# Optimization experiments

Measured on AMD Instinct MI355X. Metric: run time of the kernel, lower is better.

The kernel has to match this reference:

```python
import jax, jax.numpy as jnp
import numpy as np

N = 4096
M = 1024
APPERTURE = 250
L1, L2, L3, PRED = 1024, 512, 128, 1
EPS = 1e-6


def _layer_norm(x, gamma, beta):
    # torch x.std(-1) is unbiased (ddof=1)
    mean = jnp.mean(x, axis=-1, keepdims=True)
    std = jnp.std(x, axis=-1, ddof=1, keepdims=True)
    return gamma * (x - mean) / (std + EPS) + beta


def _self_attention(x, Wq, Wk, Wv, Wo, band_mask):
    # x: [n, m]; Linear(bias=False) => x @ W.T
    K = x @ Wk.T
    Q = (x @ Wq.T) * 0.06
    V = x @ Wv.T
    logits = Q @ K.T                      # [n, n]
    logits = jnp.where(band_mask, logits, -jnp.inf)  # keep |i-j| < apperture
    att = jax.nn.softmax(logits, axis=-1)
    # original: y = (V^T @ att)^T == att^T @ V  (note the transpose!)
    y = att.T @ V
    return y @ Wo.T, att


def setup_inputs() -> dict:
    key = jax.random.key(0)
    ks = jax.random.split(key, 20)
    s = 0.02
    inp = {
        'x1': jax.random.normal(ks[0], (1, N, M), jnp.float32),
        'x2': jax.random.normal(ks[1], (1, N, M), jnp.float32),
        'x3': jax.random.normal(ks[2], (1, N, M), jnp.float32),
        'Wq': jax.random.normal(ks[3], (M, M), jnp.float32) * s,
        'Wk': jax.random.normal(ks[4], (M, M), jnp.float32) * s,
        'Wv': jax.random.normal(ks[5], (M, M), jnp.float32) * s,
        'Wo': jax.random.normal(ks[6], (M, M), jnp.float32) * s,
        'ka_w': jax.random.normal(ks[7], (L1, M), jnp.float32) * s,
        'ka_b': jnp.zeros((L1,), jnp.float32),
        'kb_w': jax.random.normal(ks[8], (L2, L1), jnp.float32) * s,
        'kb_b': jnp.zeros((L2,), jnp.float32),
        'kc_w': jax.random.normal(ks[9], (L3, L2), jnp.float32) * s,
        'kc_b': jnp.zeros((L3,), jnp.float32),
        'kd_w': jax.random.normal(ks[10], (PRED, L3), jnp.float32) * s,
        'kd_b': jnp.zeros((PRED,), jnp.float32),
        'g13': jnp.ones((M,), jnp.float32),
        'b13': jnp.zeros((M,), jnp.float32),
        'gkc': jnp.ones((L3,), jnp.float32),
        'bkc': jnp.zeros((L3,), jnp.float32),
        'seq_len': N,
    }
    return inp


def reference(x1, x2, x3, Wq, Wk, Wv, Wo, ka_w, ka_b, kb_w, kb_b, kc_w, kc_b,
              kd_w, kd_b, g13, b13, gkc, bkc, seq_len):
    x1 = x1.reshape(-1, x1.shape[2])
    x2 = x2.reshape(-1, x2.shape[2])
    x3 = x3.reshape(-1, x3.shape[2])
    n = x1.shape[0]
    idx = jnp.arange(n)
    band_mask = jnp.abs(idx[:, None] - idx[None, :]) < APPERTURE  # allowed

    y1, att1 = _self_attention(x1, Wq, Wk, Wv, Wo, band_mask)
    y2, _ = _self_attention(x2, Wq, Wk, Wv, Wo, band_mask)
    y3, _ = _self_attention(x3, Wq, Wk, Wv, Wo, band_mask)

    # residual + (dropout == identity in eval) + shared LayerNorm
    y1 = _layer_norm(y1 + x1, g13, b13)
    y2 = _layer_norm(y2 + x2, g13, b13)
    y3 = _layer_norm(y3 + x3, g13, b13)

    y = y1 + y2 + y3  # cmb == [1,1,1]
    y = y @ ka_w.T + ka_b
    y = y @ kb_w.T + kb_b
    y = jax.nn.relu(y @ kc_w.T + kc_b)
    y = _layer_norm(y, gkc, bkc)
    y = jax.nn.sigmoid(y @ kd_w.T + kd_b)
    return y.reshape(1, -1), att1
```

## Files before the change

### kernel.cpp

```cpp
#include <hip/hip_runtime.h>
#include <hip/hip_bf16.h>
#include <cstdint>
#include <cstddef>

#define NSEQ 4096
#define MDIM 1024

typedef __attribute__((ext_vector_type(8))) short short8;
typedef __attribute__((ext_vector_type(4))) float f32x4;
typedef __attribute__((ext_vector_type(2))) long long2v;
typedef __attribute__((ext_vector_type(8))) int int8v;
typedef __attribute__((ext_vector_type(4))) int int4v;

typedef const __attribute__((address_space(1))) void gvoid_t;
typedef __attribute__((address_space(3))) void lvoid_t;

__device__ __forceinline__ unsigned short f2b(float x) {
  union { float f; unsigned int u; } a; a.f = x;
  unsigned int r = (a.u + 0x7fffu + ((a.u >> 16) & 1u)) >> 16;
  return (unsigned short)r;
}
__device__ __forceinline__ float b2f(unsigned short u) {
  union { float f; unsigned int u32; } a; a.u32 = ((unsigned int)u) << 16;
  return a.f;
}
__device__ __forceinline__ unsigned char f2e4(float x) {
  return (unsigned char)(__builtin_amdgcn_cvt_pk_fp8_f32(x, x, 0, false) & 0xff);
}
__device__ __forceinline__ unsigned int f2e4x4(float a, float b, float c, float d) {
  unsigned int lo = __builtin_amdgcn_cvt_pk_fp8_f32(a, b, 0, false);
  return (unsigned int)__builtin_amdgcn_cvt_pk_fp8_f32(c, d, lo, true);
}

__device__ __forceinline__ int8v pack32(const unsigned char* p0,
                                        const unsigned char* p1) {
  int4v lo = *(const int4v*)p0;
  int4v hi = *(const int4v*)p1;
  int8v r;
  r[0] = lo[0]; r[1] = lo[1]; r[2] = lo[2]; r[3] = lo[3];
  r[4] = hi[0]; r[5] = hi[1]; r[6] = hi[2]; r[7] = hi[3];
  return r;
}

__device__ __forceinline__ void xcd_decode(int bid, int& bx, int& by) {
  int slot = bid >> 3;
  bx = (bid & 7) * 12 + slot % 12;
  by = slot / 12;
}

__global__ __launch_bounds__(256) void k_cvt_all(
    const float* __restrict__ s0, const float* __restrict__ s1,
    const float* __restrict__ s2, const float* __restrict__ s3,
    const float* __restrict__ s4, const float* __restrict__ s5,
    const float* __restrict__ s6,
    const float* __restrict__ xa, const float* __restrict__ xb,
    const float* __restrict__ xc,
    unsigned char* __restrict__ Wf8, unsigned short* __restrict__ Wmlp,
    unsigned char* __restrict__ Xdst, float* __restrict__ sums) {
  int idx = blockIdx.x * 256 + threadIdx.x;
  if (idx < 1048576) {
    int seg = idx >> 18, local = idx & 262143;
    const float* src = (seg == 0) ? s0 : (seg == 1) ? s1 : (seg == 2) ? s2 : s3;
    float4 v = *(const float4*)(src + (size_t)local * 4);
    *(unsigned int*)(Wf8 + (size_t)idx * 4) =
        f2e4x4(v.x * 64.f, v.y * 64.f, v.z * 64.f, v.w * 64.f);
  } else if (idx < 1458176) {
    int i2 = idx - 1048576;
    const float* src; int local;
    if (i2 < 262144) { src = s4; local = i2; }
    else if (i2 < 393216) { src = s5; local = i2 - 262144; }
    else { src = s6; local = i2 - 393216; }
    float4 v = *(const float4*)(src + (size_t)local * 4);
    ushort4 o; o.x = f2b(v.x); o.y = f2b(v.y); o.z = f2b(v.z); o.w = f2b(v.w);
    *(ushort4*)(Wmlp + (size_t)i2 * 4) = o;
  } else if (idx < 4603904) {
    int i2 = idx - 1458176;
    int seg = i2 >> 20, local = i2 & 1048575;
    const float* src = (seg == 0) ? xa : (seg == 1) ? xb : xc;
    float4 v = *(const float4*)(src + (size_t)local * 4);
    *(unsigned int*)(Xdst + (size_t)i2 * 4) = f2e4x4(v.x, v.y, v.z, v.w);
  } else {
    int i3 = idx - 4603904;
    *(float4*)(sums + (size_t)i3 * 4) = make_float4(0.f, 0.f, 0.f, 0.f);
  }
}

template <int MODE, int OKIND, int DO_EXP>
__device__ __forceinline__ void gemm_core256(
    int bx, int by,
    const unsigned char* __restrict__ A, int lda,
    const unsigned char* __restrict__ B, int ldb,
    void* __restrict__ Cout, void* __restrict__ Cout2, int ldc,
    int K, float alpha,
    const unsigned char* __restrict__ A1, const unsigned char* __restrict__ A2,
    float* __restrict__ sums_out, unsigned char* __restrict__ smem) {
  const unsigned char* Ab;
  const unsigned char* Bb;
  void* Cdst = Cout;
  int ldce = ldc;
  int rbase, cbase;
  int ldae = lda, ldbe = ldb;
  if constexpr (MODE == 0) {
    Ab = A + (size_t)by * 128 * lda;
    Bb = B + (size_t)bx * 128 * ldb;
    rbase = bx * 128; cbase = by * 128;
  } else if constexpr (MODE == 3) {
    if (by < 16) {
      Ab = A + (size_t)by * 128 * lda;
      Bb = B + (size_t)bx * 128 * ldb;
      if (by >= 8) Cdst = Cout2;
      rbase = bx * 128; cbase = (by & 7) * 128;
    } else {
      Ab = B + (size_t)bx * 128 * ldb;
      Bb = A1 + (size_t)(by - 16) * 128 * 1024;
      Cdst = (void*)const_cast<unsigned char*>(A2);
      rbase = (by - 16) * 128; cbase = bx * 128;
      ldce = 3 * NSEQ;
    }
  } else {
    int s = bx >> 5, ti = bx & 31;
    int bt = ti + by - 2;
    Ab = A + (size_t)(s * 32 + bt) * 128 * lda;
    Bb = B + (size_t)bx * 128 * ldb;
    rbase = bx * 128; cbase = by * 128;
  }

  const int t = threadIdx.x;
  const int l = t & 63;
  const int w = t >> 6;
  const int fr = l & 15;
  const int quad = l >> 4;
  const int wm = (w >> 1) * 64;
  const int wn = (w & 1) * 64;
  const int fq4 = quad * 4;

  int srow[8], scg[8], sloff[8];
#pragma unroll
  for (int j = 0; j < 8; j++) {
    srow[j] = w * 32 + j * 4 + (l >> 4);
    scg[j] = ((l & 15) - srow[j]) & 15;
    sloff[j] = (w * 32 + j * 4) * 256 + l * 16;
  }

  unsigned char* As = smem;
  unsigned char* Bs = smem + 32768;

  f32x4 acc[4][4];
#pragma unroll
  for (int m = 0; m < 4; m++)
#pragma unroll
    for (int n = 0; n < 4; n++) acc[m][n] = (f32x4){0.f, 0.f, 0.f, 0.f};

  const int nt = K >> 8;
  for (int tt = 0; tt < nt; tt++) {
    int kk = tt * 256;
    __syncthreads();
#pragma unroll
    for (int j = 0; j < 8; j++)
      __builtin_amdgcn_global_load_lds(
          (gvoid_t*)(Ab + (size_t)srow[j] * ldae + kk + scg[j] * 16),
          (lvoid_t*)(As + sloff[j]), 16, 0, 0);
#pragma unroll
    for (int j = 0; j < 8; j++)
      __builtin_amdgcn_global_load_lds(
          (gvoid_t*)(Bb + (size_t)srow[j] * ldbe + kk + scg[j] * 16),
          (lvoid_t*)(Bs + sloff[j]), 16, 0, 0);
    __syncthreads();
#pragma unroll
    for (int h = 0; h < 2; h++) {
      const int cb = h * 8 + quad * 2;
      int8v a8[4], b8[4];
#pragma unroll
      for (int m = 0; m < 4; m++) {
        int r = wm + m * 16 + fr;
        int s0i = (cb + r) & 15, s1i = (cb + 1 + r) & 15;
        a8[m] = pack32(As + r * 256 + s0i * 16, As + r * 256 + s1i * 16);
      }
#pragma unroll
      for (int n = 0; n < 4; n++) {
        int r = wn + n * 16 + fr;
        int s0i = (cb + r) & 15, s1i = (cb + 1 + r) & 15;
        b8[n] = pack32(Bs + r * 256 + s0i * 16, Bs + r * 256 + s1i * 16);
      }
#pragma unroll
      for (int m = 0; m < 4; m++)
#pragma unroll
        for (int n = 0; n < 4; n++)
          acc[m][n] = __builtin_amdgcn_mfma_scale_f32_16x16x128_f8f6f4(
              a8[m], b8[n], acc[m][n], 0, 0, 0, 0x7F7F7F7F, 0, 0x7F7F7F7F);
    }
  }

  float rowsum[4] = {0.f, 0.f, 0.f, 0.f};
  const int jb = ((bx & 31) - 2) * 128;
#pragma unroll
  for (int m = 0; m < 4; m++) {
#pragma unroll
    for (int n = 0; n < 4; n++) {
      int oc = cbase + wm + m * 16 + fq4;
      int orow = rbase + wn + n * 16 + fr;
      float v0 = acc[m][n][0] * alpha, v1 = acc[m][n][1] * alpha;
      float v2 = acc[m][n][2] * alpha, v3 = acc[m][n][3] * alpha;
      if constexpr (OKIND == 1) {
        if constexpr (DO_EXP) {
          v0 = __expf(v0); v1 = __expf(v1); v2 = __expf(v2); v3 = __expf(v3);
          if constexpr (MODE == 1) {
            int d0 = (orow & 4095) - (jb + oc);
            rowsum[n] += ((unsigned)(d0 + 249) < 499u ? v0 : 0.f)
                       + ((unsigned)(d0 + 248) < 499u ? v1 : 0.f)
                       + ((unsigned)(d0 + 247) < 499u ? v2 : 0.f)
                       + ((unsigned)(d0 + 246) < 499u ? v3 : 0.f);
          }
        }
        ushort4 o; o.x = f2b(v0); o.y = f2b(v1); o.z = f2b(v2); o.w = f2b(v3);
        *(uint2*)((unsigned short*)Cdst + (size_t)orow * ldce + oc) = *(uint2*)&o;
      } else {
        *(unsigned int*)((unsigned char*)Cdst + (size_t)orow * ldce + oc) =
            f2e4x4(v0, v1, v2, v3);
      }
    }
  }
  if constexpr (MODE == 1 && DO_EXP) {
#pragma unroll
    for (int n = 0; n < 4; n++) {
      float sv = rowsum[n];
      sv += __shfl_xor(sv, 16);
      sv += __shfl_xor(sv, 32);
      if (quad == 0) {
        int orow = rbase + wn + n * 16 + fr;
        atomicAdd(sums_out + orow, sv);
      }
    }
  }
}

__device__ __forceinline__ void gemm_core_av(
    int bx, int by,
    const unsigned char* __restrict__ A, int lda,
    const unsigned char* __restrict__ B,
    void* __restrict__ Cout, int ldc, float alpha,
    const unsigned char* __restrict__ A1, const unsigned char* __restrict__ A2,
    unsigned char* __restrict__ smem) {
  int s = bx >> 5, ti = bx & 31;
  const unsigned char* Ab = A + (size_t)by * 128 * lda + s * NSEQ;
  const unsigned char* Bbase = (s == 0) ? B : ((s == 1) ? A1 : A2);
  const unsigned char* Bb = Bbase + (size_t)ti * 128 * 640;
  const int ldbe = 640;
  int lo = ti - 2; if (lo < 0) lo = 0;
  int hi = ti + 3; if (hi > 32) hi = 32;
  int k0 = lo * 128, k1 = hi * 128;
  int b_koff = (ti - 2) * 128;
  int rbase = bx * 128, cbase = by * 128;

  const int t = threadIdx.x;
  const int l = t & 63;
  const int w = t >> 6;
  const int fr = l & 15;
  const int quad = l >> 4;
  const int wm = (w >> 1) * 64;
  const int wn = (w & 1) * 64;
  const int fq4 = quad * 4;

  int srow[4], scg[4], sloff[4];
#pragma unroll
  for (int j = 0; j < 4; j++) {
    srow[j] = w * 32 + j * 8 + (l >> 3);
    scg[j] = ((l & 7) - srow[j]) & 7;
    sloff[j] = (w * 32 + j * 8) * 128 + l * 16;
  }

  f32x4 acc[4][4];
#pragma unroll
  for (int m = 0; m < 4; m++)
#pragma unroll
    for (int n = 0; n < 4; n++) acc[m][n] = (f32x4){0.f, 0.f, 0.f, 0.f};

  const int c0 = quad * 2;
  const int nt = (k1 - k0) >> 7;

  {
    int kk = k0, kb = kk - b_koff;
#pragma unroll
    for (int j = 0; j < 4; j++)
      __builtin_amdgcn_global_load_lds(
          (gvoid_t*)(Ab + (size_t)srow[j] * lda + kk + scg[j] * 16),
          (lvoid_t*)(smem + sloff[j]), 16, 0, 0);
#pragma unroll
    for (int j = 0; j < 4; j++)
      __builtin_amdgcn_global_load_lds(
          (gvoid_t*)(Bb + (size_t)srow[j] * ldbe + kb + scg[j] * 16),
          (lvoid_t*)(smem + 16384 + sloff[j]), 16, 0, 0);
  }

  for (int tt = 0; tt < nt; tt++) {
    if (tt + 1 < nt) {
      int kk = k0 + (tt + 1) * 128, kb = kk - b_koff;
      unsigned char* Asn = smem + ((tt + 1) & 1) * 32768;
#pragma unroll
      for (int j = 0; j < 4; j++)
        __builtin_amdgcn_global_load_lds(
            (gvoid_t*)(Ab + (size_t)srow[j] * lda + kk + scg[j] * 16),
            (lvoid_t*)(Asn + sloff[j]), 16, 0, 0);
#pragma unroll
      for (int j = 0; j < 4; j++)
        __builtin_amdgcn_global_load_lds(
            (gvoid_t*)(Bb + (size_t)srow[j] * ldbe + kb + scg[j] * 16),
            (lvoid_t*)(Asn + 16384 + sloff[j]), 16, 0, 0);
      __builtin_amdgcn_sched_barrier(0);
      asm volatile("s_waitcnt vmcnt(8)" ::: "memory");
    } else {
      asm volatile("s_waitcnt vmcnt(0)" ::: "memory");
    }
    asm volatile("s_barrier" ::: "memory");

    const unsigned char* Asc = smem + (tt & 1) * 32768;
    const unsigned char* Bsc = Asc + 16384;
    int8v a8[4], b8[4];
#pragma unroll
    for (int m = 0; m < 4; m++) {
      int r = wm + m * 16 + fr;
      int s0i = (c0 + r) & 7, s1i = (s0i + 1) & 7;
      a8[m] = pack32(Asc + r * 128 + s0i * 16, Asc + r * 128 + s1i * 16);
    }
#pragma unroll
    for (int n = 0; n < 4; n++) {
      int r = wn + n * 16 + fr;
      int s0i = (c0 + r) & 7, s1i = (s0i + 1) & 7;
      b8[n] = pack32(Bsc + r * 128 + s0i * 16, Bsc + r * 128 + s1i * 16);
    }
#pragma unroll
    for (int m = 0; m < 4; m++)
#pragma unroll
      for (int n = 0; n < 4; n++)
        acc[m][n] = __builtin_amdgcn_mfma_scale_f32_16x16x128_f8f6f4(
            a8[m], b8[n], acc[m][n], 0, 0, 0, 0x7F7F7F7F, 0, 0x7F7F7F7F);
    asm volatile("s_barrier" ::: "memory");
  }

#pragma unroll
  for (int m = 0; m < 4; m++) {
#pragma unroll
    for (int n = 0; n < 4; n++) {
      int oc = cbase + wm + m * 16 + fq4;
      int orow = rbase + wn + n * 16 + fr;
      float v0 = acc[m][n][0] * alpha, v1 = acc[m][n][1] * alpha;
      float v2 = acc[m][n][2] * alpha, v3 = acc[m][n][3] * alpha;
      *(unsigned int*)((unsigned char*)Cout + (size_t)orow * ldc + oc) =
          f2e4x4(v0, v1, v2, v3);
    }
  }
}

__global__ __launch_bounds__(256) void k_qkv(
    const unsigned char* __restrict__ A, const unsigned char* __restrict__ B,
    void* __restrict__ Cout, void* __restrict__ Cout2, float alpha,
    const unsigned char* __restrict__ A1, const unsigned char* __restrict__ A2) {
  __shared__ unsigned char smem[2 * 128 * 256];
  int bx, by; xcd_decode(blockIdx.x, bx, by);
  gemm_core256<3, 2, 0>(bx, by, A, 1024, B, 1024, Cout, Cout2, 1024, 1024, alpha,
                        A1, A2, nullptr, smem);
}

__global__ __launch_bounds__(256) void k_logits(
    const unsigned char* __restrict__ A, const unsigned char* __restrict__ B,
    void* __restrict__ Cout, float alpha, float* __restrict__ sums) {
  int bx, by; xcd_decode(blockIdx.x, bx, by);
  int ti = bx & 31;
  int bt = ti + by - 2;
  if (bt < 0 || bt >= 32) return;
  __shared__ unsigned char smem[2 * 128 * 256];
  gemm_core256<1, 1, 1>(bx, by, A, 1024, B, 1024, Cout, nullptr, 640, 1024, alpha,
                        nullptr, nullptr, sums, smem);
}

__global__ __launch_bounds__(256) void k_av(
    const unsigned char* __restrict__ A, const unsigned char* __restrict__ B,
    void* __restrict__ Cout, float alpha,
    const unsigned char* __restrict__ A1, const unsigned char* __restrict__ A2) {
  __shared__ unsigned char smem[4 * 128 * 128];
  int bx, by; xcd_decode(blockIdx.x, bx, by);
  gemm_core_av(bx, by, A, 3 * NSEQ, B, Cout, 1024, alpha, A1, A2, smem);
}

__global__ __launch_bounds__(256) void k_wo(
    const unsigned char* __restrict__ A, const unsigned char* __restrict__ B,
    void* __restrict__ Cout, float alpha) {
  __shared__ unsigned char smem[2 * 128 * 256];
  int bx, by; xcd_decode(blockIdx.x, bx, by);
  gemm_core256<0, 1, 0>(bx, by, A, 1024, B, 1024, Cout, nullptr, 1024, 1024, alpha,
                        nullptr, nullptr, nullptr, smem);
}

__global__ __launch_bounds__(256) void k_gemm64(
    const unsigned short* __restrict__ A, int lda,
    const unsigned short* __restrict__ B, int ldb,
    void* __restrict__ Cout, int ldc, int K,
    const float* __restrict__ bias, int relu, int out_bf16) {
  __shared__ unsigned short smem[4 * 64 * 64];
  int bx = blockIdx.x, by = blockIdx.y;
  const unsigned short* Ab = A + (size_t)by * 64 * lda;
  const unsigned short* Bb = B + (size_t)bx * 64 * ldb;
  int rbase = bx * 64, cbase = by * 64;

  const int t = threadIdx.x;
  const int l = t & 63;
  const int w = t >> 6;
  const int fr = l & 15;
  const int quad = l >> 4;
  const int wm = (w & 1) * 32;
  const int wn = (w >> 1) * 32;
  const int fq4 = quad * 4;

  int srow[2], scg[2], sloff[2];
#pragma unroll
  for (int j = 0; j < 2; j++) {
    srow[j] = w * 16 + j * 8 + (l >> 3);
    scg[j] = ((l & 7) - srow[j]) & 7;
    sloff[j] = (w * 16 + j * 8) * 64 + l * 8;
  }

  f32x4 acc[2][2];
#pragma unroll
  for (int m = 0; m < 2; m++)
#pragma unroll
    for (int n = 0; n < 2; n++) acc[m][n] = (f32x4){0.f, 0.f, 0.f, 0.f};

  const int nt = K >> 6;

#pragma unroll
  for (int j = 0; j < 2; j++)
    __builtin_amdgcn_global_load_lds(
        (gvoid_t*)(Ab + (size_t)srow[j] * lda + scg[j] * 8),
        (lvoid_t*)(smem + sloff[j]), 16, 0, 0);
#pragma unroll
  for (int j = 0; j < 2; j++)
    __builtin_amdgcn_global_load_lds(
        (gvoid_t*)(Bb + (size_t)srow[j] * ldb + scg[j] * 8),
        (lvoid_t*)(smem + 4096 + sloff[j]), 16, 0, 0);

  for (int tt = 0; tt < nt; tt++) {
    __syncthreads();
    if (tt + 1 < nt) {
      int kk = (tt + 1) * 64;
      unsigned short* Asn = smem + ((tt + 1) & 1) * 8192;
#pragma unroll
      for (int j = 0; j < 2; j++)
        __builtin_amdgcn_global_load_lds(
            (gvoid_t*)(Ab + (size_t)srow[j] * lda + kk + scg[j] * 8),
            (lvoid_t*)(Asn + sloff[j]), 16, 0, 0);
#pragma unroll
      for (int j = 0; j < 2; j++)
        __builtin_amdgcn_global_load_lds(
            (gvoid_t*)(Bb + (size_t)srow[j] * ldb + kk + scg[j] * 8),
            (lvoid_t*)(Asn + 4096 + sloff[j]), 16, 0, 0);
    }
    const unsigned short* Asc = smem + (tt & 1) * 8192;
    const unsigned short* Bsc = Asc + 4096;
#pragma unroll
    for (int s = 0; s < 2; s++) {
      short8 af[2], bf[2];
#pragma unroll
      for (int m = 0; m < 2; m++) {
        int r = wm + m * 16 + fr;
        int slot = (s * 4 + quad + r) & 7;
        af[m] = *(const short8*)(Asc + r * 64 + slot * 8);
      }
#pragma unroll
      for (int n = 0; n < 2; n++) {
        int r = wn + n * 16 + fr;
        int slot = (s * 4 + quad + r) & 7;
        bf[n] = *(const short8*)(Bsc + r * 64 + slot * 8);
      }
#pragma unroll
      for (int m = 0; m < 2; m++)
#pragma unroll
        for (int n = 0; n < 2; n++)
          acc[m][n] = __builtin_amdgcn_mfma_f32_16x16x32_bf16(af[m], bf[n], acc[m][n], 0, 0, 0);
    }
  }

#pragma unroll
  for (int m = 0; m < 2; m++) {
#pragma unroll
    for (int n = 0; n < 2; n++) {
      int oc = cbase + wm + m * 16 + fq4;
      int orow = rbase + wn + n * 16 + fr;
      float4 bv = bias ? *(const float4*)(bias + oc) : make_float4(0.f, 0.f, 0.f, 0.f);
      float v0 = acc[m][n][0] + bv.x, v1 = acc[m][n][1] + bv.y;
      float v2 = acc[m][n][2] + bv.z, v3 = acc[m][n][3] + bv.w;
      if (relu) {
        v0 = fmaxf(v0, 0.f); v1 = fmaxf(v1, 0.f);
        v2 = fmaxf(v2, 0.f); v3 = fmaxf(v3, 0.f);
      }
      if (out_bf16) {
        ushort4 o; o.x = f2b(v0); o.y = f2b(v1); o.z = f2b(v2); o.w = f2b(v3);
        *(uint2*)((unsigned short*)Cout + (size_t)orow * ldc + oc) = *(uint2*)&o;
      } else {
        *(float4*)((float*)Cout + (size_t)orow * ldc + oc) = make_float4(v0, v1, v2, v3);
      }
    }
  }
}

__global__ __launch_bounds__(256) void k_attw(const unsigned short* __restrict__ Eband,
                                              const float* __restrict__ sums,
                                              unsigned char* __restrict__ t0,
                                              unsigned char* __restrict__ t1,
                                              unsigned char* __restrict__ t2,
                                              float* __restrict__ att) {
  __shared__ unsigned char T[128][132];
  int bid = blockIdx.x;
  if (bid < 480) {
    int tjoff = bid % 5;
    int byy = bid / 5;
    int s = byy >> 5, ti = byy & 31;
    int tj = ti + tjoff - 2;
    if (tj < 0 || tj >= 32) return;
    unsigned char* dst = (s == 0) ? t0 : ((s == 1) ? t1 : t2);
    int t = threadIdx.x;
    int c0 = (ti - tj + 2) * 128;
    int colg = (t & 31) * 4;
    for (int jj = t >> 5; jj < 128; jj += 8) {
      int jg = s * NSEQ + tj * 128 + jj;
      float inv = 16.f / sums[jg];
      ushort4 v = *(const ushort4*)&Eband[(size_t)jg * 640 + c0 + colg];
      float vv[4] = {b2f(v.x), b2f(v.y), b2f(v.z), b2f(v.w)};
#pragma unroll
      for (int q = 0; q < 4; q++) {
        int i = ti * 128 + colg + q;
        int d = i - (tj * 128 + jj);
        float a = (d < 250 && d > -250) ? vv[q] * inv : 0.f;
        T[colg + q][jj] = f2e4(a);
      }
    }
    __syncthreads();
    int jb0 = (tj - ti + 2) * 128;
    for (int ii = t >> 5; ii < 128; ii += 8) {
      size_t o = (size_t)(ti * 128 + ii) * 640 + jb0 + colg;
      *(unsigned int*)(dst + o) = *(const unsigned int*)&T[ii][colg];
    }
  } else {
    int i = bid - 480;
    int ti = i >> 7, cbase = (ti - 2) * 128;
    int jlo = i - 249; if (jlo < 0) jlo = 0;
    int jhi = i + 249; if (jhi > NSEQ - 1) jhi = NSEQ - 1;
    float inv = 1.f / sums[i];
    const unsigned short* L = Eband + (size_t)i * 640;
    float* arow = att + (size_t)i * NSEQ;
    for (int j0 = threadIdx.x * 4; j0 < NSEQ; j0 += 1024) {
      float ov[4];
#pragma unroll
      for (int q = 0; q < 4; q++) {
        int j = j0 + q;
        ov[q] = (j >= jlo && j <= jhi) ? b2f(L[j - cbase]) * inv : 0.f;
      }
      *(float4*)(arow + j0) = make_float4(ov[0], ov[1], ov[2], ov[3]);
    }
  }
}

__global__ __launch_bounds__(256) void k_ln3(const unsigned short* __restrict__ yo,
                                             const float* __restrict__ x1,
                                             const float* __restrict__ x2,
                                             const float* __restrict__ x3,
                                             const float* __restrict__ g,
                                             const float* __restrict__ b,
                                             unsigned short* __restrict__ ysum_b) {
  int i = blockIdx.x, t = threadIdx.x;
  int w = t >> 6, lane = t & 63;
  __shared__ float red[8];
  const float* xs[3] = {x1, x2, x3};
  float4 gg = *(const float4*)(g + t * 4);
  float4 bb = *(const float4*)(b + t * 4);
  float acc[4] = {0.f, 0.f, 0.f, 0.f};
  for (int s = 0; s < 3; s++) {
    ushort4 yv = *(const ushort4*)(yo + ((size_t)(s * NSEQ + i)) * MDIM + t * 4);
    float4 xx = *(const float4*)(xs[s] + (size_t)i * MDIM + t * 4);
    float v[4] = {b2f(yv.x) + xx.x, b2f(yv.y) + xx.y, b2f(yv.z) + xx.z, b2f(yv.w) + xx.w};
    float s1 = v[0] + v[1] + v[2] + v[3];
    float s2 = v[0]*v[0] + v[1]*v[1] + v[2]*v[2] + v[3]*v[3];
    for (int off = 32; off; off >>= 1) { s1 += __shfl_xor(s1, off); s2 += __shfl_xor(s2, off); }
    __syncthreads();
    if (lane == 0) { red[w] = s1; red[4 + w] = s2; }
    __syncthreads();
    float S1 = red[0] + red[1] + red[2] + red[3];
    float S2 = red[4] + red[5] + red[6] + red[7];
    float mean = S1 * (1.f / 1024.f);
    float var = (S2 - S1 * mean) * (1.f / 1023.f);
    float rstd = 1.f / (sqrtf(var) + 1e-6f);
    acc[0] += gg.x * (v[0] - mean) * rstd + bb.x;
    acc[1] += gg.y * (v[1] - mean) * rstd + bb.y;
    acc[2] += gg.z * (v[2] - mean) * rstd + bb.z;
    acc[3] += gg.w * (v[3] - mean) * rstd + bb.w;
  }
  ushort4 o;
  o.x = f2b(acc[0]); o.y = f2b(acc[1]); o.z = f2b(acc[2]); o.w = f2b(acc[3]);
  *(ushort4*)(ysum_b + (size_t)i * MDIM + t * 4) = o;
}

__global__ __launch_bounds__(128) void k_final(const float* __restrict__ h3,
                                               const float* __restrict__ g,
                                               const float* __restrict__ b,
                                               const float* __restrict__ kdw,
                                               const float* __restrict__ kdb,
                                               float* __restrict__ yout) {
  int i = blockIdx.x, t = threadIdx.x;
  float v = h3[(size_t)i * 128 + t];
  float s1 = v, s2 = v * v;
  for (int off = 32; off; off >>= 1) { s1 += __shfl_xor(s1, off); s2 += __shfl_xor(s2, off); }
  __shared__ float red[4];
  int w = t >> 6, lane = t & 63;
  if (lane == 0) { red[w] = s1; red[2 + w] = s2; }
  __syncthreads();
  float S1 = red[0] + red[1], S2 = red[2] + red[3];
  float mean = S1 * (1.f / 128.f);
  float var = (S2 - S1 * mean) * (1.f / 127.f);
  float rstd = 1.f / (sqrtf(var) + 1e-6f);
  float ln = g[t] * (v - mean) * rstd + b[t];
  float p = ln * kdw[t];
  for (int off = 32; off; off >>= 1) p += __shfl_xor(p, off);
  __syncthreads();
  if (lane == 0) red[w] = p;
  __syncthreads();
  if (t == 0) {
    float z = red[0] + red[1] + kdb[0];
    yout[i] = 1.f / (1.f + __expf(-z));
  }
}

extern "C" void kernel_launch(void* const* d_in, const int* in_sizes, int n_in,
                              void* d_out, int out_size, void* d_ws, size_t ws_size,
                              hipStream_t stream) {
  const float* x1 = (const float*)d_in[0];
  const float* x2 = (const float*)d_in[1];
  const float* x3 = (const float*)d_in[2];
  const float* Wq = (const float*)d_in[3];
  const float* Wk = (const float*)d_in[4];
  const float* Wv = (const float*)d_in[5];
  const float* Wo = (const float*)d_in[6];
  const float* ka_w = (const float*)d_in[7];
  const float* ka_b = (const float*)d_in[8];
  const float* kb_w = (const float*)d_in[9];
  const float* kb_b = (const float*)d_in[10];
  const float* kc_w = (const float*)d_in[11];
  const float* kc_b = (const float*)d_in[12];
  const float* kd_w = (const float*)d_in[13];
  const float* kd_b = (const float*)d_in[14];
  const float* g13 = (const float*)d_in[15];
  const float* b13 = (const float*)d_in[16];
  const float* gkc = (const float*)d_in[17];
  const float* bkc = (const float*)d_in[18];

  float* y_out = (float*)d_out;
  float* att_out = y_out + NSEQ;

  char* ws = (char*)d_ws;
  size_t off = 0;
  auto alloc = [&](size_t bytes) -> void* {
    void* p = ws + off;
    off += (bytes + 255) & ~(size_t)255;
    return p;
  };
  const size_t NM = (size_t)3 * NSEQ * MDIM;
  unsigned char* Wf = (unsigned char*)alloc(4 * 1048576);
  unsigned short* Wmlp = (unsigned short*)alloc((1048576 + 524288 + 65536) * 2);
  unsigned char* Xf = (unsigned char*)alloc(NM);
  unsigned char* Qf = (unsigned char*)alloc(NM);
  unsigned char* Kf = (unsigned char*)alloc(NM);
  unsigned char* VTf = (unsigned char*)alloc(NM);
  unsigned short* Eband = (unsigned short*)alloc((size_t)3 * NSEQ * 640 * 2);
  float* sums = (float*)alloc((size_t)3 * NSEQ * 4);
  unsigned char* aT0 = (unsigned char*)alloc((size_t)NSEQ * 640);
  unsigned char* aT1 = (unsigned char*)alloc((size_t)NSEQ * 640);
  unsigned char* aT2 = (unsigned char*)alloc((size_t)NSEQ * 640);
  unsigned char* Wv_f = Wf + 2097152;
  unsigned char* Wo_f = Wf + 3145728;
  unsigned short* ka_b16 = Wmlp;
  unsigned short* kb_b16 = Wmlp + 1048576;
  unsigned short* kc_b16 = Wmlp + 1572864;
  unsigned char* yb = Xf;
  unsigned short* yo = (unsigned short*)Qf;
  unsigned short* ysum_b = (unsigned short*)VTf;
  unsigned short* h1b = (unsigned short*)Xf;
  unsigned short* h2b = (unsigned short*)Qf;
  float* h3 = (float*)aT0;

  k_cvt_all<<<17996, 256, 0, stream>>>(Wq, Wk, Wv, Wo, ka_w, kb_w, kc_w,
                                       x1, x2, x3, Wf, Wmlp, Xf, sums);

  k_qkv<<<2304, 256, 0, stream>>>(Wf, Xf, Qf, Kf, 1.f / 64.f, Wv_f, VTf);
  k_logits<<<480, 256, 0, stream>>>(Kf, Qf, Eband, 0.06f, sums);
  k_attw<<<4576, 256, 0, stream>>>(Eband, sums, aT0, aT1, aT2, att_out);
  k_av<<<768, 256, 0, stream>>>(VTf, aT0, yb, 0.5f, aT1, aT2);
  k_wo<<<768, 256, 0, stream>>>(Wo_f, yb, yo, 1.f / 512.f);
  k_ln3<<<4096, 256, 0, stream>>>(yo, x1, x2, x3, g13, b13, ysum_b);

  k_gemm64<<<dim3(64, 16), 256, 0, stream>>>(ka_b16, 1024, ysum_b, 1024, h1b, 1024,
                                             1024, ka_b, 0, 1);
  k_gemm64<<<dim3(64, 8), 256, 0, stream>>>(kb_b16, 1024, h1b, 1024, h2b, 512,
                                            1024, kb_b, 0, 1);
  k_gemm64<<<dim3(64, 2), 256, 0, stream>>>(kc_b16, 512, h2b, 512, h3, 128,
                                            512, kc_b, 1, 0);
  k_final<<<4096, 128, 0, stream>>>(h3, gkc, bkc, kd_w, kd_b, y_out);
}
```

Measured before the change: 315.0 us.

## Fuse Q/K and V-pair projections into dual-accumulator kernel sharing the X tile

Replaces the generic QKV GEMM with a dedicated kernel where each block loads one X tile and two weight tiles (Wq+Wk, or two Wv row blocks), computing two output tiles with two accumulator sets. This halves the block count and reuses the shared X tile across two MFMA streams to cut global and LDS traffic. The MLP GEMM launches also get an XCD-aware block-index remap for better L2 locality. The cost is doubled accumulator registers, which may reduce occupancy, and a smaller K step (128) with more barriers.

```diff
diff --git a/kernel.cpp b/kernel.cpp
--- a/kernel.cpp
+++ b/kernel.cpp
@@ -85,44 +85,28 @@
   }
 }
 
-template <int MODE, int OKIND, int DO_EXP>
-__device__ __forceinline__ void gemm_core256(
-    int bx, int by,
-    const unsigned char* __restrict__ A, int lda,
-    const unsigned char* __restrict__ B, int ldb,
-    void* __restrict__ Cout, void* __restrict__ Cout2, int ldc,
-    int K, float alpha,
-    const unsigned char* __restrict__ A1, const unsigned char* __restrict__ A2,
-    float* __restrict__ sums_out, unsigned char* __restrict__ smem) {
-  const unsigned char* Ab;
-  const unsigned char* Bb;
-  void* Cdst = Cout;
-  int ldce = ldc;
-  int rbase, cbase;
-  int ldae = lda, ldbe = ldb;
-  if constexpr (MODE == 0) {
-    Ab = A + (size_t)by * 128 * lda;
-    Bb = B + (size_t)bx * 128 * ldb;
-    rbase = bx * 128; cbase = by * 128;
-  } else if constexpr (MODE == 3) {
-    if (by < 16) {
-      Ab = A + (size_t)by * 128 * lda;
-      Bb = B + (size_t)bx * 128 * ldb;
-      if (by >= 8) Cdst = Cout2;
-      rbase = bx * 128; cbase = (by & 7) * 128;
-    } else {
-      Ab = B + (size_t)bx * 128 * ldb;
-      Bb = A1 + (size_t)(by - 16) * 128 * 1024;
-      Cdst = (void*)const_cast<unsigned char*>(A2);
-      rbase = (by - 16) * 128; cbase = bx * 128;
-      ldce = 3 * NSEQ;
-    }
+__global__ __launch_bounds__(256) void k_qkv(
+    const unsigned char* __restrict__ W, const unsigned char* __restrict__ X,
+    unsigned char* __restrict__ Qf, unsigned char* __restrict__ Kf,
+    unsigned char* __restrict__ VT, float alpha) {
+  __shared__ unsigned char smem[3 * 128 * 128];
+  unsigned char* S  = smem;
+  unsigned char* U1 = smem + 16384;
+  unsigned char* U2 = smem + 32768;
+  int slot = blockIdx.x >> 3;
+  int bx = (blockIdx.x & 7) * 12 + slot % 12;
+  int by = slot / 12;
+  const bool qk = (by < 8);
+  const unsigned char* Sb = X + (size_t)bx * 128 * 1024;
+  const unsigned char* U1b;
+  const unsigned char* U2b;
+  if (qk) {
+    U1b = W + (size_t)by * 131072;
+    U2b = W + 1048576 + (size_t)by * 131072;
   } else {
-    int s = bx >> 5, ti = bx & 31;
-    int bt = ti + by - 2;
-    Ab = A + (size_t)(s * 32 + bt) * 128 * lda;
-    Bb = B + (size_t)bx * 128 * ldb;
-    rbase = bx * 128; cbase = by * 128;
+    int j = by - 8;
+    U1b = W + 2097152 + (size_t)j * 131072;
+    U2b = W + 2097152 + (size_t)(j + 4) * 131072;
   }
 
   const int t = threadIdx.x;
@@ -134,6 +118,187 @@
   const int wn = (w & 1) * 64;
   const int fq4 = quad * 4;
 
+  int srow[4], scg[4], sloff[4];
+#pragma unroll
+  for (int j = 0; j < 4; j++) {
+    srow[j] = w * 32 + j * 8 + (l >> 3);
+    scg[j] = ((l & 7) - srow[j]) & 7;
+    sloff[j] = (w * 32 + j * 8) * 128 + l * 16;
+  }
+
+  f32x4 acc1[4][4], acc2[4][4];
+#pragma unroll
+  for (int m = 0; m < 4; m++)
+#pragma unroll
+    for (int n = 0; n < 4; n++) {
+      acc1[m][n] = (f32x4){0.f, 0.f, 0.f, 0.f};
+      acc2[m][n] = (f32x4){0.f, 0.f, 0.f, 0.f};
+    }
+
+  const int c0 = quad * 2;
+  for (int tt = 0; tt < 8; tt++) {
+    int kk = tt * 128;
+    __syncthreads();
+#pragma unroll
+    for (int j = 0; j < 4; j++)
+      __builtin_amdgcn_global_load_lds(
+          (gvoid_t*)(Sb + (size_t)srow[j] * 1024 + kk + scg[j] * 16),
+          (lvoid_t*)(S + sloff[j]), 16, 0, 0);
+#pragma unroll
+    for (int j = 0; j < 4; j++)
+      __builtin_amdgcn_global_load_lds(
+          (gvoid_t*)(U1b + (size_t)srow[j] * 1024 + kk + scg[j] * 16),
+          (lvoid_t*)(U1 + sloff[j]), 16, 0, 0);
+#pragma unroll
+    for (int j = 0; j < 4; j++)
+      __builtin_amdgcn_global_load_lds(
+          (gvoid_t*)(U2b + (size_t)srow[j] * 1024 + kk + scg[j] * 16),
+          (lvoid_t*)(U2 + sloff[j]), 16, 0, 0);
+    __syncthreads();
+    if (qk) {
+      int8v b8[4];
+#pragma unroll
+      for (int n = 0; n < 4; n++) {
+        int r = wn + n * 16 + fr;
+        int s0i = (c0 + r) & 7, s1i = (s0i + 1) & 7;
+        b8[n] = pack32(S + r * 128 + s0i * 16, S + r * 128 + s1i * 16);
+      }
+      {
+        int8v a8[4];
+#pragma unroll
+        for (int m = 0; m < 4; m++) {
+          int r = wm + m * 16 + fr;
+          int s0i = (c0 + r) & 7, s1i = (s0i + 1) & 7;
+          a8[m] = pack32(U1 + r * 128 + s0i * 16, U1 + r * 128 + s1i * 16);
+        }
+#pragma unroll
+        for (int m = 0; m < 4; m++)
+#pragma unroll
+          for (int n = 0; n < 4; n++)
+            acc1[m][n] = __builtin_amdgcn_mfma_scale_f32_16x16x128_f8f6f4(
+                a8[m], b8[n], acc1[m][n], 0, 0, 0, 0x7F7F7F7F, 0, 0x7F7F7F7F);
+#pragma unroll
+        for (int m = 0; m < 4; m++) {
+          int r = wm + m * 16 + fr;
+          int s0i = (c0 + r) & 7, s1i = (s0i + 1) & 7;
+          a8[m] = pack32(U2 + r * 128 + s0i * 16, U2 + r * 128 + s1i * 16);
+        }
+#pragma unroll
+        for (int m = 0; m < 4; m++)
+#pragma unroll
+          for (int n = 0; n < 4; n++)
+            acc2[m][n] = __builtin_amdgcn_mfma_scale_f32_16x16x128_f8f6f4(
+                a8[m], b8[n], acc2[m][n], 0, 0, 0, 0x7F7F7F7F, 0, 0x7F7F7F7F);
+      }
+    } else {
+      int8v a8[4];
+#pragma unroll
+      for (int m = 0; m < 4; m++) {
+        int r = wm + m * 16 + fr;
+        int s0i = (c0 + r) & 7, s1i = (s0i + 1) & 7;
+        a8[m] = pack32(S + r * 128 + s0i * 16, S + r * 128 + s1i * 16);
+      }
+      {
+        int8v b8[4];
+#pragma unroll
+        for (int n = 0; n < 4; n++) {
+          int r = wn + n * 16 + fr;
+          int s0i = (c0 + r) & 7, s1i = (s0i + 1) & 7;
+          b8[n] = pack32(U1 + r * 128 + s0i * 16, U1 + r * 128 + s1i * 16);
+        }
+#pragma unroll
+        for (int m = 0; m < 4; m++)
+#pragma unroll
+          for (int n = 0; n < 4; n++)
+            acc1[m][n] = __builtin_amdgcn_mfma_scale_f32_16x16x128_f8f6f4(
+                a8[m], b8[n], acc1[m][n], 0, 0, 0, 0x7F7F7F7F, 0, 0x7F7F7F7F);
+#pragma unroll
+        for (int n = 0; n < 4; n++) {
+          int r = wn + n * 16 + fr;
+          int s0i = (c0 + r) & 7, s1i = (s0i + 1) & 7;
+          b8[n] = pack32(U2 + r * 128 + s0i * 16, U2 + r * 128 + s1i * 16);
+        }
+#pragma unroll
+        for (int m = 0; m < 4; m++)
+#pragma unroll
+          for (int n = 0; n < 4; n++)
+            acc2[m][n] = __builtin_amdgcn_mfma_scale_f32_16x16x128_f8f6f4(
+                a8[m], b8[n], acc2[m][n], 0, 0, 0, 0x7F7F7F7F, 0, 0x7F7F7F7F);
+      }
+    }
+  }
+
+  if (qk) {
+    int cbase = by * 128, rbase = bx * 128;
+#pragma unroll
+    for (int m = 0; m < 4; m++) {
+#pragma unroll
+      for (int n = 0; n < 4; n++) {
+        int oc = cbase + wm + m * 16 + fq4;
+        int orow = rbase + wn + n * 16 + fr;
+        *(unsigned int*)(Qf + (size_t)orow * 1024 + oc) =
+            f2e4x4(acc1[m][n][0] * alpha, acc1[m][n][1] * alpha,
+                   acc1[m][n][2] * alpha, acc1[m][n][3] * alpha);
+        *(unsigned int*)(Kf + (size_t)orow * 1024 + oc) =
+            f2e4x4(acc2[m][n][0] * alpha, acc2[m][n][1] * alpha,
+                   acc2[m][n][2] * alpha, acc2[m][n][3] * alpha);
+      }
+    }
+  } else {
+    int j = by - 8;
+    int cbase = bx * 128;
+    int rb1 = j * 128, rb2 = (j + 4) * 128;
+#pragma unroll
+    for (int m = 0; m < 4; m++) {
+#pragma unroll
+      for (int n = 0; n < 4; n++) {
+        int oc = cbase + wm + m * 16 + fq4;
+        int oro = wn + n * 16 + fr;
+        *(unsigned int*)(VT + (size_t)(rb1 + oro) * 12288 + oc) =
+            f2e4x4(acc1[m][n][0] * alpha, acc1[m][n][1] * alpha,
+                   acc1[m][n][2] * alpha, acc1[m][n][3] * alpha);
+        *(unsigned int*)(VT + (size_t)(rb2 + oro) * 12288 + oc) =
+            f2e4x4(acc2[m][n][0] * alpha, acc2[m][n][1] * alpha,
+                   acc2[m][n][2] * alpha, acc2[m][n][3] * alpha);
+      }
+    }
+  }
+}
+
+template <int MODE, int OKIND, int DO_EXP>
+__device__ __forceinline__ void gemm_core256(
+    int bx, int by,
+    const unsigned char* __restrict__ A, int lda,
+    const unsigned char* __restrict__ B, int ldb,
+    void* __restrict__ Cout, int ldc,
+    int K, float alpha,
+    float* __restrict__ sums_out, unsigned char* __restrict__ smem) {
+  const unsigned char* Ab;
+  const unsigned char* Bb;
+  int ldce = ldc;
+  int rbase, cbase;
+  int ldae = lda, ldbe = ldb;
+  if constexpr (MODE == 0) {
+    Ab = A + (size_t)by * 128 * lda;
+    Bb = B + (size_t)bx * 128 * ldb;
+    rbase = bx * 128; cbase = by * 128;
+  } else {
+    int s = bx >> 5, ti = bx & 31;
+    int bt = ti + by - 2;
+    Ab = A + (size_t)(s * 32 + bt) * 128 * lda;
+    Bb = B + (size_t)bx * 128 * ldb;
+    rbase = bx * 128; cbase = by * 128;
+  }
+
+  const int t = threadIdx.x;
+  const int l = t & 63;
+  const int w = t >> 6;
+  const int fr = l & 15;
+  const int quad = l >> 4;
+  const int wm = (w >> 1) * 64;
+  const int wn = (w & 1) * 64;
+  const int fq4 = quad * 4;
+
   int srow[8], scg[8], sloff[8];
 #pragma unroll
   for (int j = 0; j < 8; j++) {
@@ -201,23 +366,18 @@
       int orow = rbase + wn + n * 16 + fr;
       float v0 = acc[m][n][0] * alpha, v1 = acc[m][n][1] * alpha;
       float v2 = acc[m][n][2] * alpha, v3 = acc[m][n][3] * alpha;
-      if constexpr (OKIND == 1) {
-        if constexpr (DO_EXP) {
-          v0 = __expf(v0); v1 = __expf(v1); v2 = __expf(v2); v3 = __expf(v3);
-          if constexpr (MODE == 1) {
-            int d0 = (orow & 4095) - (jb + oc);
-            rowsum[n] += ((unsigned)(d0 + 249) < 499u ? v0 : 0.f)
-                       + ((unsigned)(d0 + 248) < 499u ? v1 : 0.f)
-                       + ((unsigned)(d0 + 247) < 499u ? v2 : 0.f)
-                       + ((unsigned)(d0 + 246) < 499u ? v3 : 0.f);
-          }
+      if constexpr (DO_EXP) {
+        v0 = __expf(v0); v1 = __expf(v1); v2 = __expf(v2); v3 = __expf(v3);
+        if constexpr (MODE == 1) {
+          int d0 = (orow & 4095) - (jb + oc);
+          rowsum[n] += ((unsigned)(d0 + 249) < 499u ? v0 : 0.f)
+                     + ((unsigned)(d0 + 248) < 499u ? v1 : 0.f)
+                     + ((unsigned)(d0 + 247) < 499u ? v2 : 0.f)
+                     + ((unsigned)(d0 + 246) < 499u ? v3 : 0.f);
         }
-        ushort4 o; o.x = f2b(v0); o.y = f2b(v1); o.z = f2b(v2); o.w = f2b(v3);
-        *(uint2*)((unsigned short*)Cdst + (size_t)orow * ldce + oc) = *(uint2*)&o;
-      } else {
-        *(unsigned int*)((unsigned char*)Cdst + (size_t)orow * ldce + oc) =
-            f2e4x4(v0, v1, v2, v3);
-      }
+      }
+      ushort4 o; o.x = f2b(v0); o.y = f2b(v1); o.z = f2b(v2); o.w = f2b(v3);
+      *(uint2*)((unsigned short*)Cout + (size_t)orow * ldce + oc) = *(uint2*)&o;
     }
   }
   if constexpr (MODE == 1 && DO_EXP) {
@@ -351,16 +511,6 @@
   }
 }
 
-__global__ __launch_bounds__(256) void k_qkv(
-    const unsigned char* __restrict__ A, const unsigned char* __restrict__ B,
-    void* __restrict__ Cout, void* __restrict__ Cout2, float alpha,
-    const unsigned char* __restrict__ A1, const unsigned char* __restrict__ A2) {
-  __shared__ unsigned char smem[2 * 128 * 256];
-  int bx, by; xcd_decode(blockIdx.x, bx, by);
-  gemm_core256<3, 2, 0>(bx, by, A, 1024, B, 1024, Cout, Cout2, 1024, 1024, alpha,
-                        A1, A2, nullptr, smem);
-}
-
 __global__ __launch_bounds__(256) void k_logits(
     const unsigned char* __restrict__ A, const unsigned char* __restrict__ B,
     void* __restrict__ Cout, float alpha, float* __restrict__ sums) {
@@ -369,8 +519,8 @@
   int bt = ti + by - 2;
   if (bt < 0 || bt >= 32) return;
   __shared__ unsigned char smem[2 * 128 * 256];
-  gemm_core256<1, 1, 1>(bx, by, A, 1024, B, 1024, Cout, nullptr, 640, 1024, alpha,
-                        nullptr, nullptr, sums, smem);
+  gemm_core256<1, 1, 1>(bx, by, A, 1024, B, 1024, Cout, 640, 1024, alpha,
+                        sums, smem);
 }
 
 __global__ __launch_bounds__(256) void k_av(
@@ -387,8 +537,8 @@
     void* __restrict__ Cout, float alpha) {
   __shared__ unsigned char smem[2 * 128 * 256];
   int bx, by; xcd_decode(blockIdx.x, bx, by);
-  gemm_core256<0, 1, 0>(bx, by, A, 1024, B, 1024, Cout, nullptr, 1024, 1024, alpha,
-                        nullptr, nullptr, nullptr, smem);
+  gemm_core256<0, 1, 0>(bx, by, A, 1024, B, 1024, Cout, 1024, 1024, alpha,
+                        nullptr, smem);
 }
 
 __global__ __launch_bounds__(256) void k_gemm64(
@@ -397,7 +547,9 @@
     void* __restrict__ Cout, int ldc, int K,
     const float* __restrict__ bias, int relu, int out_bf16) {
   __shared__ unsigned short smem[4 * 64 * 64];
-  int bx = blockIdx.x, by = blockIdx.y;
+  int slot = blockIdx.x >> 3;
+  int bx = (blockIdx.x & 7) * 8 + (slot & 7);
+  int by = slot >> 3;
   const unsigned short* Ab = A + (size_t)by * 64 * lda;
   const unsigned short* Bb = B + (size_t)bx * 64 * ldb;
   int rbase = bx * 64, cbase = by * 64;
@@ -462,14 +614,14 @@
 #pragma unroll
       for (int m = 0; m < 2; m++) {
         int r = wm + m * 16 + fr;
-        int slot = (s * 4 + quad + r) & 7;
-        af[m] = *(const short8*)(Asc + r * 64 + slot * 8);
+        int slot2 = (s * 4 + quad + r) & 7;
+        af[m] = *(const short8*)(Asc + r * 64 + slot2 * 8);
       }
 #pragma unroll
       for (int n = 0; n < 2; n++) {
         int r = wn + n * 16 + fr;
-        int slot = (s * 4 + quad + r) & 7;
-        bf[n] = *(const short8*)(Bsc + r * 64 + slot * 8);
+        int slot2 = (s * 4 + quad + r) & 7;
+        bf[n] = *(const short8*)(Bsc + r * 64 + slot2 * 8);
       }
 #pragma unroll
       for (int m = 0; m < 2; m++)
@@ -673,7 +825,6 @@
   unsigned char* aT0 = (unsigned char*)alloc((size_t)NSEQ * 640);
   unsigned char* aT1 = (unsigned char*)alloc((size_t)NSEQ * 640);
   unsigned char* aT2 = (unsigned char*)alloc((size_t)NSEQ * 640);
-  unsigned char* Wv_f = Wf + 2097152;
   unsigned char* Wo_f = Wf + 3145728;
   unsigned short* ka_b16 = Wmlp;
   unsigned short* kb_b16 = Wmlp + 1048576;
@@ -688,18 +839,18 @@
   k_cvt_all<<<17996, 256, 0, stream>>>(Wq, Wk, Wv, Wo, ka_w, kb_w, kc_w,
                                        x1, x2, x3, Wf, Wmlp, Xf, sums);
 
-  k_qkv<<<2304, 256, 0, stream>>>(Wf, Xf, Qf, Kf, 1.f / 64.f, Wv_f, VTf);
+  k_qkv<<<1152, 256, 0, stream>>>(Wf, Xf, Qf, Kf, VTf, 1.f / 64.f);
   k_logits<<<480, 256, 0, stream>>>(Kf, Qf, Eband, 0.06f, sums);
   k_attw<<<4576, 256, 0, stream>>>(Eband, sums, aT0, aT1, aT2, att_out);
   k_av<<<768, 256, 0, stream>>>(VTf, aT0, yb, 0.5f, aT1, aT2);
   k_wo<<<768, 256, 0, stream>>>(Wo_f, yb, yo, 1.f / 512.f);
   k_ln3<<<4096, 256, 0, stream>>>(yo, x1, x2, x3, g13, b13, ysum_b);
 
-  k_gemm64<<<dim3(64, 16), 256, 0, stream>>>(ka_b16, 1024, ysum_b, 1024, h1b, 1024,
-                                             1024, ka_b, 0, 1);
-  k_gemm64<<<dim3(64, 8), 256, 0, stream>>>(kb_b16, 1024, h1b, 1024, h2b, 512,
-                                            1024, kb_b, 0, 1);
-  k_gemm64<<<dim3(64, 2), 256, 0, stream>>>(kc_b16, 512, h2b, 512, h3, 128,
-                                            512, kc_b, 1, 0);
+  k_gemm64<<<1024, 256, 0, stream>>>(ka_b16, 1024, ysum_b, 1024, h1b, 1024,
+                                     1024, ka_b, 0, 1);
+  k_gemm64<<<512, 256, 0, stream>>>(kb_b16, 1024, h1b, 1024, h2b, 512,
+                                    1024, kb_b, 0, 1);
+  k_gemm64<<<128, 256, 0, stream>>>(kc_b16, 512, h2b, 512, h3, 128,
+                                    512, kc_b, 1, 0);
   k_final<<<4096, 128, 0, stream>>>(h3, gkc, bkc, kd_w, kd_b, y_out);
 }
```

New measurement: 352.3 us. 1.12x slower.
